# Kernel tuning notes

Measured on AMD Instinct MI355X. Metric: run time of the kernel, lower is better.

## Reference

```python
import jax, jax.numpy as jnp
import numpy as np

B, SQ, SK = 2, 2048, 2048
QDIM = KDIM = HID = 1024
H = 16
DH = HID // H  # inner_dim = 64


def setup_inputs() -> dict:
    key = jax.random.key(0)
    ks = jax.random.split(key, 8)
    q = jax.random.normal(ks[0], (B, SQ, QDIM), dtype=jnp.float32)
    k = jax.random.normal(ks[1], (B, SK, KDIM), dtype=jnp.float32)
    v = jax.random.normal(ks[2], (B, SK, KDIM), dtype=jnp.float32)
    mask = jax.random.randint(ks[3], (B, SQ, SK), 0, 2).astype(jnp.bool_)
    scale = 1.0 / np.sqrt(QDIM)
    # per-head projections, stored stacked: [H, in_dim, DH]
    Wq = jax.random.normal(ks[4], (H, QDIM, DH), dtype=jnp.float32) * scale
    Wk = jax.random.normal(ks[5], (H, KDIM, DH), dtype=jnp.float32) * scale
    Wv = jax.random.normal(ks[6], (H, KDIM, DH), dtype=jnp.float32) * scale
    Wo = jax.random.normal(ks[7], (HID, QDIM), dtype=jnp.float32) * scale
    return {"q": q, "k": k, "v": v, "mask": mask,
            "Wq": Wq, "Wk": Wk, "Wv": Wv, "Wo": Wo}


def reference(q, k, v, mask, Wq, Wk, Wv, Wo):
    dh = Wq.shape[-1]
    qh = jnp.einsum('bsd,hde->bhse', q, Wq)   # [B,H,SQ,DH]
    kh = jnp.einsum('bsd,hde->bhse', k, Wk)   # [B,H,SK,DH]
    vh = jnp.einsum('bsd,hde->bhse', v, Wv)   # [B,H,SK,DH]
    scores = jnp.einsum('bhqd,bhkd->bhqk', qh, kh) / jnp.sqrt(jnp.asarray(dh, qh.dtype))
    scores = jnp.where(mask[:, None, :, :], -jnp.inf, scores)
    attn = jax.nn.softmax(scores, axis=-1)
    att = jnp.einsum('bhqk,bhkd->bhqd', attn, vh)        # [B,H,SQ,DH]
    concat = att.transpose(0, 2, 1, 3).reshape(q.shape[0], q.shape[1], -1)  # head-order concat
    return concat @ Wo  # [B,SQ,QDIM]
```

## Files before the change

### kernel.cpp

```cpp
#include <hip/hip_runtime.h>

#define NB 2
#define NH 16
#define SEQ 2048
#define DMODEL 1024
#define DHEAD 64
#define QSCALE 0.18033688f

typedef __attribute__((ext_vector_type(8))) short bf16x8;
typedef __attribute__((ext_vector_type(4))) short bf16x4;
typedef __attribute__((ext_vector_type(4))) float f32x4;
typedef __attribute__((ext_vector_type(16))) float f32x16;
typedef __attribute__((ext_vector_type(4))) int i32x4;

static __device__ __forceinline__ unsigned short f2bf(float f) {
    unsigned int u = __float_as_uint(f);
    u += 0x7fffu + ((u >> 16) & 1u);
    return (unsigned short)(u >> 16);
}
static __device__ __forceinline__ unsigned int pk2(float lo, float hi) {
    return (unsigned int)f2bf(lo) | ((unsigned int)f2bf(hi) << 16);
}
static __device__ __forceinline__ void gld_lds16(const unsigned short* g, unsigned short* l) {
    __builtin_amdgcn_global_load_lds(
        (const __attribute__((address_space(1))) unsigned int*)g,
        (__attribute__((address_space(3))) unsigned int*)l, 16, 0, 0);
}

__global__ __launch_bounds__(256) void prep_kernel(
    const int* __restrict__ mask, unsigned long long* __restrict__ mpack,
    const float* __restrict__ Wq, const float* __restrict__ Wk, const float* __restrict__ Wv,
    unsigned short* __restrict__ Wqt, unsigned short* __restrict__ Wkt,
    unsigned short* __restrict__ Wvt,
    const float* __restrict__ Wo, unsigned short* __restrict__ Wot,
    const float* __restrict__ q, const float* __restrict__ k, const float* __restrict__ v,
    unsigned short* __restrict__ qb, unsigned short* __restrict__ kb,
    unsigned short* __restrict__ vb)
{
    __shared__ __align__(16) float Ls[64][65];
    const int bid = blockIdx.x, t = threadIdx.x;

    if (bid < 1024) {
        const int wave = bid * 4 + (t >> 6);
        const int lane = t & 63;
        const int* row = mask + (size_t)wave * SEQ;
        unsigned long long* orow = mpack + (size_t)wave * (SEQ / 64);
        for (int w = 0; w < SEQ / 64; ++w) {
            int m = row[w * 64 + lane];
            unsigned long long bits = __ballot(m != 0);
            if (lane == 0) orow[w] = bits;
        }
    } else if (bid < 2048) {
        const float* S; unsigned short* D; float scale; int R, tile_r, tile_c, ostride;
        if (bid < 1792) {
            const int local = bid - 1024, z = local >> 4, sel = z >> 4, h = z & 15;
            S = (sel == 0 ? Wq : sel == 1 ? Wk : Wv) + (size_t)h * DMODEL * DHEAD;
            D = (sel == 0 ? Wqt : sel == 1 ? Wkt : Wvt) + (size_t)h * DMODEL * DHEAD;
            scale = (sel == 0) ? QSCALE : 1.0f;
            tile_r = (local & 15) * 64; tile_c = 0; R = DHEAD; ostride = DMODEL;
        } else {
            const int local = bid - 1792;
            S = Wo; D = Wot; scale = 1.0f;
            tile_c = (local & 15) * 64; tile_r = (local >> 4) * 64; R = DMODEL; ostride = DMODEL;
        }
        const int c4 = (t & 15) * 4;
        for (int rr = t >> 4; rr < 64; rr += 16) {
            float4 x = *(const float4*)(S + (size_t)(tile_r + rr) * R + tile_c + c4);
            Ls[rr][c4 + 0] = x.x; Ls[rr][c4 + 1] = x.y;
            Ls[rr][c4 + 2] = x.z; Ls[rr][c4 + 3] = x.w;
        }
        __syncthreads();
        const int r4 = (t & 15) * 4;
        for (int cc = t >> 4; cc < 64; cc += 16) {
            ushort4 o;
            o.x = f2bf(Ls[r4 + 0][cc] * scale); o.y = f2bf(Ls[r4 + 1][cc] * scale);
            o.z = f2bf(Ls[r4 + 2][cc] * scale); o.w = f2bf(Ls[r4 + 3][cc] * scale);
            *(ushort4*)(D + (size_t)(tile_c + cc) * ostride + tile_r + r4) = o;
        }
    } else {
        const int local = bid - 2048;
        const int z = local >> 11;
        const float* S = (z == 0) ? q : (z == 1) ? k : v;
        unsigned short* D = (z == 0) ? qb : (z == 1) ? kb : vb;
        const size_t i = ((size_t)(local & 2047) * 256 + t) * 8;
        float4 x0 = *(const float4*)(S + i);
        float4 x1 = *(const float4*)(S + i + 4);
        uint4 val;
        val.x = pk2(x0.x, x0.y); val.y = pk2(x0.z, x0.w);
        val.z = pk2(x1.x, x1.y); val.w = pk2(x1.z, x1.w);
        *(uint4*)(D + i) = val;
    }
}

__global__ __launch_bounds__(256) void proj_gemm_kernel(
    const unsigned short* __restrict__ qb, const unsigned short* __restrict__ kb,
    const unsigned short* __restrict__ vb,
    const unsigned short* __restrict__ Wqt, const unsigned short* __restrict__ Wkt,
    const unsigned short* __restrict__ Wvt,
    unsigned short* __restrict__ qh, unsigned short* __restrict__ kh,
    unsigned short* __restrict__ vt)
{
    const int bid = blockIdx.x;
    const int sx = bid >> 3;
    const int mtg = (bid & 7) * 12 + (sx >> 3);
    const int z = mtg >> 5;
    const int m0 = (mtg & 31) * 128;
    const int n0 = (sx & 7) * 128;

    const unsigned short* A = (z == 0) ? qb : (z == 1) ? kb : vb;
    const unsigned short* Bt = (z == 0) ? Wqt : (z == 1) ? Wkt : Wvt;

    const int t = threadIdx.x, lane = t & 63, w = t >> 6;
    const int lg = lane >> 4, ln = lane & 15;
    const int wx = w & 1, wy = w >> 1;

    __shared__ __align__(16) unsigned short As[128 * 64];
    __shared__ __align__(16) unsigned short Bs[128 * 64];

    f32x4 acc[4][4] = {};

    for (int kk = 0; kk < DMODEL; kk += 64) {
        #pragma unroll
        for (int i = 0; i < 4; ++i) {
            int s = (w * 4 + i) * 64 + lane;
            int n = s >> 3, c = (s & 7) ^ (n & 7);
            gld_lds16(Bt + (size_t)(n0 + n) * DMODEL + kk + c * 8, Bs + (size_t)s * 8);
        }
        #pragma unroll
        for (int i = 0; i < 4; ++i) {
            int s = (w * 4 + i) * 64 + lane;
            int n = s >> 3, c = (s & 7) ^ (n & 7);
            gld_lds16(A + (size_t)(m0 + n) * DMODEL + kk + c * 8, As + (size_t)s * 8);
        }
        __syncthreads();
        #pragma unroll
        for (int ks = 0; ks < 2; ++ks) {
            bf16x8 af[4], bf[4];
            #pragma unroll
            for (int rb = 0; rb < 4; ++rb) {
                int r = wy * 64 + rb * 16 + ln;
                af[rb] = *(const bf16x8*)(As + r * 64 + (((ks * 4 + lg) ^ (r & 7)) * 8));
            }
            #pragma unroll
            for (int nb = 0; nb < 4; ++nb) {
                int n = wx * 64 + nb * 16 + ln;
                bf[nb] = *(const bf16x8*)(Bs + n * 64 + (((ks * 4 + lg) ^ (n & 7)) * 8));
            }
            #pragma unroll
            for (int rb = 0; rb < 4; ++rb)
                #pragma unroll
                for (int nb = 0; nb < 4; ++nb)
                    acc[rb][nb] = __builtin_amdgcn_mfma_f32_16x16x32_bf16(
                        af[rb], bf[nb], acc[rb][nb], 0, 0, 0);
        }
        __syncthreads();
    }

    if (z < 2) {
        unsigned short* Y = (z == 0) ? qh : kh;
        #pragma unroll
        for (int rb = 0; rb < 4; ++rb)
            #pragma unroll
            for (int nb = 0; nb < 4; ++nb)
                #pragma unroll
                for (int r = 0; r < 4; ++r) {
                    int grow = m0 + wy * 64 + rb * 16 + lg * 4 + r;
                    int gcol = n0 + wx * 64 + nb * 16 + ln;
                    size_t idx = ((size_t)((grow >> 11) * NH + (gcol >> 6)) * SEQ
                                  + (grow & (SEQ - 1))) * DHEAD + (gcol & 63);
                    Y[idx] = f2bf(acc[rb][nb][r]);
                }
    } else {
        #pragma unroll
        for (int rb = 0; rb < 4; ++rb)
            #pragma unroll
            for (int nb = 0; nb < 4; ++nb) {
                int grow0 = m0 + wy * 64 + rb * 16 + lg * 4;
                int gcol  = n0 + wx * 64 + nb * 16 + ln;
                int bh = ((grow0 >> 11) << 4) + (gcol >> 6);
                ushort4 st;
                st.x = f2bf(acc[rb][nb][0]); st.y = f2bf(acc[rb][nb][1]);
                st.z = f2bf(acc[rb][nb][2]); st.w = f2bf(acc[rb][nb][3]);
                *(ushort4*)(vt + ((size_t)bh * DHEAD + (gcol & 63)) * SEQ
                                 + (grow0 & (SEQ - 1))) = st;
            }
    }
}

__global__ __launch_bounds__(256, 2) void attn_kernel(
    const unsigned short* __restrict__ qh, const unsigned short* __restrict__ kh,
    const unsigned short* __restrict__ vt, const unsigned long long* __restrict__ mpack,
    unsigned short* __restrict__ att)
{
    const int t = threadIdx.x, lane = t & 63, w = t >> 6;
    const int h = lane >> 5, lq = lane & 31;
    const int L = lq & 7, X = (lq >> 3) & 3;

    const int bid = blockIdx.x;
    const int r_ = bid >> 3;
    const int qt = r_ & 15;
    const int bh = (bid & 7) * 4 + (r_ >> 4);
    const int b = bh >> 4, hd = bh & 15;
    const int row0 = qt * 128;
    const int qrow = row0 + w * 32 + lq;

    __shared__ __align__(16) unsigned short SMEM[4 * 64 * 64];

    const unsigned short* Kb = kh + (size_t)bh * SEQ * DHEAD;
    const unsigned short* Vb = vt + (size_t)bh * DHEAD * SEQ;

    const unsigned short* Qb = qh + ((size_t)bh * SEQ + qrow) * DHEAD;
    bf16x8 qf[4];
    #pragma unroll
    for (int d = 0; d < 4; ++d) qf[d] = *(const bf16x8*)(Qb + d * 16 + h * 8);

    const unsigned long long* Mb = mpack + ((size_t)b * SEQ + qrow) * (SEQ / 64);

    int oK[2], oV[2], sL[2];
    #pragma unroll
    for (int i = 0; i < 2; ++i) {
        const int s = i * 256 + t;
        const int n = s >> 3, c = (s & 7) ^ (n & 7) ^ ((n >> 3) & 3);
        sL[i] = s * 8;
        oK[i] = n * DHEAD + c * 8;
        oV[i] = n * SEQ + c * 8;
    }

    f32x16 acc[2] = {};
    f32x16 lacc = {};
    bf16x8 ones;
    #pragma unroll
    for (int i = 0; i < 8; ++i) ones[i] = (short)0x3f80;

    unsigned long long mw, mwn = 0;

    #pragma unroll
    for (int i = 0; i < 2; ++i)
        gld_lds16(Kb + oK[i], SMEM + sL[i]);
    #pragma unroll
    for (int i = 0; i < 2; ++i)
        gld_lds16(Vb + oV[i], SMEM + 2 * 4096 + sL[i]);
    mw = Mb[0];
    __syncthreads();

    for (int tix = 0; tix < 32; ++tix) {
        const int buf = tix & 1;

        if (tix < 31) {
            const int ktn = (tix + 1) * 64;
            unsigned short* Kd = SMEM + (buf ^ 1) * 4096;
            unsigned short* Vd = SMEM + 2 * 4096 + (buf ^ 1) * 4096;
            #pragma unroll
            for (int i = 0; i < 2; ++i)
                gld_lds16(Kb + (size_t)ktn * DHEAD + oK[i], Kd + sL[i]);
            #pragma unroll
            for (int i = 0; i < 2; ++i)
                gld_lds16(Vb + (size_t)ktn + oV[i], Vd + sL[i]);
            mwn = Mb[tix + 1];
        }

        const unsigned short* Ksb = SMEM + buf * 4096;
        const unsigned short* Vsb = SMEM + 2 * 4096 + buf * 4096;
        const unsigned long long mh_ = mw >> (h * 4);

        #pragma unroll
        for (int st = 0; st < 2; ++st) {
            f32x16 S = {};
            #pragma unroll
            for (int d = 0; d < 4; ++d) {
                bf16x8 kf = *(const bf16x8*)(Ksb + (st * 32 + lq) * 64
                                             + (((d * 2 + h) ^ L ^ X) * 8));
                S = __builtin_amdgcn_mfma_f32_32x32x16_bf16(kf, qf[d], S, 0, 0, 0);
            }
            const int sb = 32 * st;
            unsigned int pd[8];
            #pragma unroll
            for (int bb = 0; bb < 4; ++bb) {
                float e[4];
                #pragma unroll
                for (int rr = 0; rr < 4; ++rr) {
                    const bool m = (mh_ >> (sb + 8 * bb + rr)) & 1ull;
                    float ex = __builtin_amdgcn_exp2f(S[bb * 4 + rr]);
                    e[rr] = m ? 0.0f : ex;
                }
                pd[bb * 2 + 0] = __builtin_amdgcn_perm(
                    __float_as_uint(e[1]), __float_as_uint(e[0]), 0x07060302u);
                pd[bb * 2 + 1] = __builtin_amdgcn_perm(
                    __float_as_uint(e[3]), __float_as_uint(e[2]), 0x07060302u);
            }
            #pragma unroll
            for (int k2 = 0; k2 < 2; ++k2) {
                i32x4 pi = { (int)pd[4 * k2 + 0], (int)pd[4 * k2 + 1],
                             (int)pd[4 * k2 + 2], (int)pd[4 * k2 + 3] };
                bf16x8 pf = __builtin_bit_cast(bf16x8, pi);
                lacc = __builtin_amdgcn_mfma_f32_32x32x16_bf16(ones, pf, lacc, 0, 0, 0);
                const int p0 = (((4 * st + 2 * k2) ^ L ^ X)) * 8;
                #pragma unroll
                for (int dt = 0; dt < 2; ++dt) {
                    const unsigned short* vb_ = Vsb + (dt * 32 + lq) * 64 + 4 * h;
                    bf16x4 v0 = *(const bf16x4*)(vb_ + p0);
                    bf16x4 v1 = *(const bf16x4*)(vb_ + (p0 ^ 8));
                    bf16x8 vf = __builtin_shufflevector(v0, v1, 0, 1, 2, 3, 4, 5, 6, 7);
                    acc[dt] = __builtin_amdgcn_mfma_f32_32x32x16_bf16(vf, pf, acc[dt], 0, 0, 0);
                }
            }
        }

        mw = mwn;
        __syncthreads();
    }

    const float linv = 1.0f / lacc[0];
    unsigned short* Ar = att + ((size_t)b * SEQ + qrow) * DMODEL + hd * DHEAD;
    #pragma unroll
    for (int dt = 0; dt < 2; ++dt)
        #pragma unroll
        for (int g = 0; g < 4; ++g) {
            const int dh0 = dt * 32 + 8 * g + 4 * h;
            ushort4 o;
            o.x = f2bf(acc[dt][g * 4 + 0] * linv);
            o.y = f2bf(acc[dt][g * 4 + 1] * linv);
            o.z = f2bf(acc[dt][g * 4 + 2] * linv);
            o.w = f2bf(acc[dt][g * 4 + 3] * linv);
            *(ushort4*)(Ar + dh0) = o;
        }
}

__global__ __launch_bounds__(256) void out_gemm_kernel(
    const unsigned short* __restrict__ A, const unsigned short* __restrict__ Bt,
    float* __restrict__ C)
{
    const int bid = blockIdx.x;
    const int sx = bid >> 3;
    const int m0 = ((bid & 7) * 4 + (sx >> 3)) * 128;
    const int n0 = (sx & 7) * 128;

    const int t = threadIdx.x, lane = t & 63, w = t >> 6;
    const int lg = lane >> 4, ln = lane & 15;
    const int wx = w & 1, wy = w >> 1;

    __shared__ __align__(16) unsigned short As[128 * 64];
    __shared__ __align__(16) unsigned short Bs[128 * 64];

    f32x4 acc[4][4] = {};

    for (int kk = 0; kk < DMODEL; kk += 64) {
        #pragma unroll
        for (int i = 0; i < 4; ++i) {
            int s = (w * 4 + i) * 64 + lane;
            int n = s >> 3, c = (s & 7) ^ (n & 7);
            gld_lds16(Bt + (size_t)(n0 + n) * DMODEL + kk + c * 8, Bs + (size_t)s * 8);
        }
        #pragma unroll
        for (int i = 0; i < 4; ++i) {
            int s = (w * 4 + i) * 64 + lane;
            int n = s >> 3, c = (s & 7) ^ (n & 7);
            gld_lds16(A + (size_t)(m0 + n) * DMODEL + kk + c * 8, As + (size_t)s * 8);
        }
        __syncthreads();
        #pragma unroll
        for (int ks = 0; ks < 2; ++ks) {
            bf16x8 af[4], bf[4];
            #pragma unroll
            for (int rb = 0; rb < 4; ++rb) {
                int r = wy * 64 + rb * 16 + ln;
                af[rb] = *(const bf16x8*)(As + r * 64 + (((ks * 4 + lg) ^ (r & 7)) * 8));
            }
            #pragma unroll
            for (int nb = 0; nb < 4; ++nb) {
                int n = wx * 64 + nb * 16 + ln;
                bf[nb] = *(const bf16x8*)(Bs + n * 64 + (((ks * 4 + lg) ^ (n & 7)) * 8));
            }
            #pragma unroll
            for (int rb = 0; rb < 4; ++rb)
                #pragma unroll
                for (int nb = 0; nb < 4; ++nb)
                    acc[rb][nb] = __builtin_amdgcn_mfma_f32_16x16x32_bf16(
                        af[rb], bf[nb], acc[rb][nb], 0, 0, 0);
        }
        __syncthreads();
    }

    #pragma unroll
    for (int rb = 0; rb < 4; ++rb)
        #pragma unroll
        for (int nb = 0; nb < 4; ++nb)
            #pragma unroll
            for (int r = 0; r < 4; ++r) {
                int grow = m0 + wy * 64 + rb * 16 + lg * 4 + r;
                int gcol = n0 + wx * 64 + nb * 16 + ln;
                C[(size_t)grow * DMODEL + gcol] = acc[rb][nb][r];
            }
}

extern "C" void kernel_launch(void* const* d_in, const int* in_sizes, int n_in,
                              void* d_out, int out_size, void* d_ws, size_t ws_size,
                              hipStream_t stream) {
    const float* q    = (const float*)d_in[0];
    const float* k    = (const float*)d_in[1];
    const float* v    = (const float*)d_in[2];
    const int*   mask = (const int*)  d_in[3];
    const float* Wq   = (const float*)d_in[4];
    const float* Wk   = (const float*)d_in[5];
    const float* Wv   = (const float*)d_in[6];
    const float* Wo   = (const float*)d_in[7];
    float* out = (float*)d_out;

    unsigned short* ws  = (unsigned short*)d_ws;
    const size_t n1 = (size_t)NB * NH * SEQ * DHEAD;
    const size_t nw = (size_t)NH * DHEAD * DMODEL;
    unsigned short* qh  = ws;
    unsigned short* kh  = qh + n1;
    unsigned short* vt  = kh + n1;
    unsigned short* att = vt + n1;
    unsigned short* Wqt = att + n1;
    unsigned short* Wkt = Wqt + nw;
    unsigned short* Wvt = Wkt + nw;
    unsigned short* Wot = Wvt + nw;
    unsigned long long* mpack = (unsigned long long*)(Wot + nw);
    unsigned short* regA = (unsigned short*)(mpack + (size_t)NB * SEQ * (SEQ / 64));
    unsigned short* qb = regA;
    unsigned short* kb = qb + n1;
    unsigned short* vb = kb + n1;

    prep_kernel<<<dim3(8192), 256, 0, stream>>>(
        mask, mpack, Wq, Wk, Wv, Wqt, Wkt, Wvt, Wo, Wot, q, k, v, qb, kb, vb);
    proj_gemm_kernel<<<dim3(768), 256, 0, stream>>>(qb, kb, vb, Wqt, Wkt, Wvt, qh, kh, vt);
    attn_kernel<<<dim3(512), 256, 0, stream>>>(qh, kh, vt, mpack, att);
    out_gemm_kernel<<<dim3(256), 256, 0, stream>>>(att, Wot, out);
}
```

Before: 258.7 us.

## Stage projection epilogue through LDS, widen attention K tiles, split output GEMM tiles

The projection GEMM epilogue now writes its bf16 results into shared memory first, then emits coalesced 16-byte global stores for the Q/K head layout and the transposed V layout, replacing scattered 2-byte and 8-byte stores. The attention kernel now processes 128 keys per iteration instead of 64, doubling the LDS buffers and halving the loop count and barriers, and loads two mask words at once. The output GEMM uses 64-row tiles with 512 blocks to fill more compute units. The larger attention LDS footprint (64KB) may limit occupancy against the launch bound of 2 blocks per CU.

After: 254.2 us. Within noise of the previous version (-1.7%).

```diff
diff --git a/kernel.cpp b/kernel.cpp
--- a/kernel.cpp
+++ b/kernel.cpp
@@ -114,8 +114,9 @@
     const int lg = lane >> 4, ln = lane & 15;
     const int wx = w & 1, wy = w >> 1;
 
-    __shared__ __align__(16) unsigned short As[128 * 64];
-    __shared__ __align__(16) unsigned short Bs[128 * 64];
+    __shared__ __align__(16) unsigned short SM[17408];
+    unsigned short* As = SM;
+    unsigned short* Bs = SM + 8192;
 
     f32x4 acc[4][4] = {};
 
@@ -158,32 +159,53 @@
 
     if (z < 2) {
         unsigned short* Y = (z == 0) ? qh : kh;
+        unsigned short* Ep = SM;
         #pragma unroll
         for (int rb = 0; rb < 4; ++rb)
             #pragma unroll
-            for (int nb = 0; nb < 4; ++nb)
+            for (int nb = 0; nb < 4; ++nb) {
+                const int c_l = wx * 64 + nb * 16 + ln;
+                const int base = ((c_l >> 6) << 13) + (c_l & 63);
                 #pragma unroll
                 for (int r = 0; r < 4; ++r) {
-                    int grow = m0 + wy * 64 + rb * 16 + lg * 4 + r;
-                    int gcol = n0 + wx * 64 + nb * 16 + ln;
-                    size_t idx = ((size_t)((grow >> 11) * NH + (gcol >> 6)) * SEQ
-                                  + (grow & (SEQ - 1))) * DHEAD + (gcol & 63);
-                    Y[idx] = f2bf(acc[rb][nb][r]);
+                    const int s_l = wy * 64 + rb * 16 + lg * 4 + r;
+                    Ep[base + s_l * 64] = f2bf(acc[rb][nb][r]);
                 }
+            }
+        __syncthreads();
+        {
+            const int head = t >> 7, r2 = t & 127;
+            const unsigned short* src = Ep + head * 8192 + r2 * 64;
+            unsigned short* dst = Y + ((size_t)((m0 >> 11) * NH + (n0 >> 6) + head) * SEQ
+                                       + (m0 & (SEQ - 1)) + r2) * DHEAD;
+            #pragma unroll
+            for (int i = 0; i < 8; ++i)
+                *(uint4*)(dst + i * 8) = *(const uint4*)(src + i * 8);
+        }
     } else {
+        unsigned short* Ep = SM;
         #pragma unroll
         for (int rb = 0; rb < 4; ++rb)
             #pragma unroll
             for (int nb = 0; nb < 4; ++nb) {
-                int grow0 = m0 + wy * 64 + rb * 16 + lg * 4;
-                int gcol  = n0 + wx * 64 + nb * 16 + ln;
-                int bh = ((grow0 >> 11) << 4) + (gcol >> 6);
-                ushort4 st;
-                st.x = f2bf(acc[rb][nb][0]); st.y = f2bf(acc[rb][nb][1]);
-                st.z = f2bf(acc[rb][nb][2]); st.w = f2bf(acc[rb][nb][3]);
-                *(ushort4*)(vt + ((size_t)bh * DHEAD + (gcol & 63)) * SEQ
-                                 + (grow0 & (SEQ - 1))) = st;
-            }
+                const int c_l = wx * 64 + nb * 16 + ln;
+                const int seq0 = wy * 64 + rb * 16 + lg * 4;
+                ushort4 o;
+                o.x = f2bf(acc[rb][nb][0]); o.y = f2bf(acc[rb][nb][1]);
+                o.z = f2bf(acc[rb][nb][2]); o.w = f2bf(acc[rb][nb][3]);
+                *(ushort4*)(Ep + (c_l >> 6) * 8704 + (c_l & 63) * 136 + seq0) = o;
+            }
+        __syncthreads();
+        {
+            const int head = t >> 7, dh = (t >> 1) & 63, hf = t & 1;
+            const unsigned short* src = Ep + head * 8704 + dh * 136 + hf * 64;
+            unsigned short* dst = vt
+                + ((size_t)((((m0 >> 11) << 4) + (n0 >> 6) + head) * DHEAD + dh) * SEQ
+                   + (m0 & (SEQ - 1)) + hf * 64);
+            #pragma unroll
+            for (int i = 0; i < 8; ++i)
+                *(uint4*)(dst + i * 8) = *(const uint4*)(src + i * 8);
+        }
     }
 }
 
@@ -204,7 +226,7 @@
     const int row0 = qt * 128;
     const int qrow = row0 + w * 32 + lq;
 
-    __shared__ __align__(16) unsigned short SMEM[4 * 64 * 64];
+    __shared__ __align__(16) unsigned short SMEM[4 * 8192];
 
     const unsigned short* Kb = kh + (size_t)bh * SEQ * DHEAD;
     const unsigned short* Vb = vt + (size_t)bh * DHEAD * SEQ;
@@ -216,14 +238,15 @@
 
     const unsigned long long* Mb = mpack + ((size_t)b * SEQ + qrow) * (SEQ / 64);
 
-    int oK[2], oV[2], sL[2];
-    #pragma unroll
-    for (int i = 0; i < 2; ++i) {
+    int oK[4], oV[4], sL[4];
+    #pragma unroll
+    for (int i = 0; i < 4; ++i) {
         const int s = i * 256 + t;
-        const int n = s >> 3, c = (s & 7) ^ (n & 7) ^ ((n >> 3) & 3);
         sL[i] = s * 8;
-        oK[i] = n * DHEAD + c * 8;
-        oV[i] = n * SEQ + c * 8;
+        { const int n = s >> 3, c = (s & 7) ^ (n & 7) ^ ((n >> 3) & 3);
+          oK[i] = n * DHEAD + c * 8; }
+        { const int n = s >> 4, c = (s & 15) ^ (n & 7) ^ ((n >> 3) & 3);
+          oV[i] = n * SEQ + c * 8; }
     }
 
     f32x16 acc[2] = {};
@@ -232,39 +255,40 @@
     #pragma unroll
     for (int i = 0; i < 8; ++i) ones[i] = (short)0x3f80;
 
-    unsigned long long mw, mwn = 0;
-
-    #pragma unroll
-    for (int i = 0; i < 2; ++i)
+    ulonglong2 mw, mwn;
+
+    #pragma unroll
+    for (int i = 0; i < 4; ++i)
         gld_lds16(Kb + oK[i], SMEM + sL[i]);
     #pragma unroll
-    for (int i = 0; i < 2; ++i)
-        gld_lds16(Vb + oV[i], SMEM + 2 * 4096 + sL[i]);
-    mw = Mb[0];
+    for (int i = 0; i < 4; ++i)
+        gld_lds16(Vb + oV[i], SMEM + 16384 + sL[i]);
+    mw = *(const ulonglong2*)(Mb);
     __syncthreads();
 
-    for (int tix = 0; tix < 32; ++tix) {
+    for (int tix = 0; tix < 16; ++tix) {
         const int buf = tix & 1;
 
-        if (tix < 31) {
-            const int ktn = (tix + 1) * 64;
-            unsigned short* Kd = SMEM + (buf ^ 1) * 4096;
-            unsigned short* Vd = SMEM + 2 * 4096 + (buf ^ 1) * 4096;
-            #pragma unroll
-            for (int i = 0; i < 2; ++i)
+        if (tix < 15) {
+            const int ktn = (tix + 1) * 128;
+            unsigned short* Kd = SMEM + (buf ^ 1) * 8192;
+            unsigned short* Vd = SMEM + 16384 + (buf ^ 1) * 8192;
+            #pragma unroll
+            for (int i = 0; i < 4; ++i)
                 gld_lds16(Kb + (size_t)ktn * DHEAD + oK[i], Kd + sL[i]);
             #pragma unroll
-            for (int i = 0; i < 2; ++i)
+            for (int i = 0; i < 4; ++i)
                 gld_lds16(Vb + (size_t)ktn + oV[i], Vd + sL[i]);
-            mwn = Mb[tix + 1];
-        }
-
-        const unsigned short* Ksb = SMEM + buf * 4096;
-        const unsigned short* Vsb = SMEM + 2 * 4096 + buf * 4096;
-        const unsigned long long mh_ = mw >> (h * 4);
-
-        #pragma unroll
-        for (int st = 0; st < 2; ++st) {
+            mwn = *(const ulonglong2*)(Mb + (size_t)(tix + 1) * 2);
+        }
+
+        const unsigned short* Ksb = SMEM + buf * 8192;
+        const unsigned short* Vsb = SMEM + 16384 + buf * 8192;
+        const unsigned long long mh0 = mw.x >> (h * 4);
+        const unsigned long long mh1 = mw.y >> (h * 4);
+
+        #pragma unroll
+        for (int st = 0; st < 4; ++st) {
             f32x16 S = {};
             #pragma unroll
             for (int d = 0; d < 4; ++d) {
@@ -272,14 +296,15 @@
                                              + (((d * 2 + h) ^ L ^ X) * 8));
                 S = __builtin_amdgcn_mfma_f32_32x32x16_bf16(kf, qf[d], S, 0, 0, 0);
             }
-            const int sb = 32 * st;
+            const unsigned long long mh = (st < 2) ? mh0 : mh1;
+            const int sb = 32 * (st & 1);
             unsigned int pd[8];
             #pragma unroll
             for (int bb = 0; bb < 4; ++bb) {
                 float e[4];
                 #pragma unroll
                 for (int rr = 0; rr < 4; ++rr) {
-                    const bool m = (mh_ >> (sb + 8 * bb + rr)) & 1ull;
+                    const bool m = (mh >> (sb + 8 * bb + rr)) & 1ull;
                     float ex = __builtin_amdgcn_exp2f(S[bb * 4 + rr]);
                     e[rr] = m ? 0.0f : ex;
                 }
@@ -297,7 +322,7 @@
                 const int p0 = (((4 * st + 2 * k2) ^ L ^ X)) * 8;
                 #pragma unroll
                 for (int dt = 0; dt < 2; ++dt) {
-                    const unsigned short* vb_ = Vsb + (dt * 32 + lq) * 64 + 4 * h;
+                    const unsigned short* vb_ = Vsb + (dt * 32 + lq) * 128 + 4 * h;
                     bf16x4 v0 = *(const bf16x4*)(vb_ + p0);
                     bf16x4 v1 = *(const bf16x4*)(vb_ + (p0 ^ 8));
                     bf16x8 vf = __builtin_shufflevector(v0, v1, 0, 1, 2, 3, 4, 5, 6, 7);
@@ -332,17 +357,17 @@
 {
     const int bid = blockIdx.x;
     const int sx = bid >> 3;
-    const int m0 = ((bid & 7) * 4 + (sx >> 3)) * 128;
+    const int m0 = ((bid & 7) * 8 + (sx >> 3)) * 64;
     const int n0 = (sx & 7) * 128;
 
     const int t = threadIdx.x, lane = t & 63, w = t >> 6;
     const int lg = lane >> 4, ln = lane & 15;
     const int wx = w & 1, wy = w >> 1;
 
-    __shared__ __align__(16) unsigned short As[128 * 64];
+    __shared__ __align__(16) unsigned short As[64 * 64];
     __shared__ __align__(16) unsigned short Bs[128 * 64];
 
-    f32x4 acc[4][4] = {};
+    f32x4 acc[2][4] = {};
 
     for (int kk = 0; kk < DMODEL; kk += 64) {
         #pragma unroll
@@ -352,18 +377,18 @@
             gld_lds16(Bt + (size_t)(n0 + n) * DMODEL + kk + c * 8, Bs + (size_t)s * 8);
         }
         #pragma unroll
-        for (int i = 0; i < 4; ++i) {
-            int s = (w * 4 + i) * 64 + lane;
+        for (int i = 0; i < 2; ++i) {
+            int s = (w * 2 + i) * 64 + lane;
             int n = s >> 3, c = (s & 7) ^ (n & 7);
             gld_lds16(A + (size_t)(m0 + n) * DMODEL + kk + c * 8, As + (size_t)s * 8);
         }
         __syncthreads();
         #pragma unroll
         for (int ks = 0; ks < 2; ++ks) {
-            bf16x8 af[4], bf[4];
-            #pragma unroll
-            for (int rb = 0; rb < 4; ++rb) {
-                int r = wy * 64 + rb * 16 + ln;
+            bf16x8 af[2], bf[4];
+            #pragma unroll
+            for (int rb = 0; rb < 2; ++rb) {
+                int r = wy * 32 + rb * 16 + ln;
                 af[rb] = *(const bf16x8*)(As + r * 64 + (((ks * 4 + lg) ^ (r & 7)) * 8));
             }
             #pragma unroll
@@ -372,7 +397,7 @@
                 bf[nb] = *(const bf16x8*)(Bs + n * 64 + (((ks * 4 + lg) ^ (n & 7)) * 8));
             }
             #pragma unroll
-            for (int rb = 0; rb < 4; ++rb)
+            for (int rb = 0; rb < 2; ++rb)
                 #pragma unroll
                 for (int nb = 0; nb < 4; ++nb)
                     acc[rb][nb] = __builtin_amdgcn_mfma_f32_16x16x32_bf16(
@@ -382,12 +407,12 @@
     }
 
     #pragma unroll
-    for (int rb = 0; rb < 4; ++rb)
+    for (int rb = 0; rb < 2; ++rb)
         #pragma unroll
         for (int nb = 0; nb < 4; ++nb)
             #pragma unroll
             for (int r = 0; r < 4; ++r) {
-                int grow = m0 + wy * 64 + rb * 16 + lg * 4 + r;
+                int grow = m0 + wy * 32 + rb * 16 + lg * 4 + r;
                 int gcol = n0 + wx * 64 + nb * 16 + ln;
                 C[(size_t)grow * DMODEL + gcol] = acc[rb][nb][r];
             }
@@ -427,5 +452,5 @@
         mask, mpack, Wq, Wk, Wv, Wqt, Wkt, Wvt, Wo, Wot, q, k, v, qb, kb, vb);
     proj_gemm_kernel<<<dim3(768), 256, 0, stream>>>(qb, kb, vb, Wqt, Wkt, Wvt, qh, kh, vt);
     attn_kernel<<<dim3(512), 256, 0, stream>>>(qh, kh, vt, mpack, att);
-    out_gemm_kernel<<<dim3(256), 256, 0, stream>>>(att, Wot, out);
-}
+    out_gemm_kernel<<<dim3(512), 256, 0, stream>>>(att, Wot, out);
+}
```
